# Optimization experiments

Measured on AMD Instinct MI355X. Metric: run time of the kernel, lower is better.

## Reference

```python
import jax, jax.numpy as jnp
import numpy as np

N, M, L, D = 8, 32, 256, 768
H = 4 * D  # mlp hidden
EPS = 1e-5


def setup_inputs() -> dict:
    key = jax.random.key(0)
    ks = jax.random.split(key, 8)
    s = 0.02
    return {
        "x": jax.random.normal(ks[0], (N, M, L, D), jnp.float32),
        "probe": jax.random.normal(ks[1], (1, 1, 1, D), jnp.float32) * s,
        "wq": jax.random.normal(ks[2], (D, D), jnp.float32) * s,
        "bq": jnp.zeros((D,), jnp.float32),
        "wk": jax.random.normal(ks[3], (D, D), jnp.float32) * s,
        "bk": jnp.zeros((D,), jnp.float32),
        "wv": jax.random.normal(ks[4], (D, D), jnp.float32) * s,
        "bv": jnp.zeros((D,), jnp.float32),
        "gamma": jnp.ones((D,), jnp.float32),
        "beta": jnp.zeros((D,), jnp.float32),
        "w1": jax.random.normal(ks[5], (H, D), jnp.float32) * s,
        "b1": jnp.zeros((H,), jnp.float32),
        "w2": jax.random.normal(ks[6], (D, H), jnp.float32) * s,
        "b2": jnp.zeros((D,), jnp.float32),
    }


def _layernorm(x, gamma, beta):
    mu = jnp.mean(x, axis=-1, keepdims=True)
    var = jnp.var(x, axis=-1, keepdims=True)
    return (x - mu) * jax.lax.rsqrt(var + EPS) * gamma + beta


def reference(x, probe, wq, bq, wk, bk, wv, bv, gamma, beta, w1, b1, w2, b2):
    n, m, l, d = x.shape
    # probe is tiled over (n, m); the query projection is identical per (n, m),
    # so compute it once: (1,1,q,d) -> (q,d)
    q = probe[0, 0] @ wq.T + bq                      # (q, d)
    k = x @ wk.T + bk                                # (n, m, l, d)
    v = x @ wv.T + bv                                # (n, m, l, d)
    att = jnp.einsum('qd,nmkd->nmqk', q, k)          # (n, m, q, l)
    att = jax.nn.softmax(att / jnp.sqrt(jnp.float32(d)), axis=-1)
    xo = jnp.einsum('nmqk,nmkd->nmqd', att, v)       # (n, m, q, d)
    y = _layernorm(xo, gamma, beta)
    h = jax.nn.gelu(y @ w1.T + b1, approximate=False)
    out = xo + (h @ w2.T + b2)
    return out[:, :, 0, :]                           # (n, m, d)
```

## Files before the change

### kernel.cpp

```cpp
#include <hip/hip_runtime.h>
#include <math.h>

#define D_ 768
#define H_ 3072
#define L_ 256
#define NM_ 256
#define EPS_ 1e-5f
#define SCALE_ 0.036084391824351615f

__device__ __forceinline__ float wave_sum(float v) {
#pragma unroll
  for (int o = 32; o; o >>= 1) v += __shfl_down(v, o);
  return v;
}

__global__ __launch_bounds__(256) void k_qproj(const float* __restrict__ probe,
                                               const float* __restrict__ wq,
                                               const float* __restrict__ bq,
                                               float* __restrict__ q_out) {
  __shared__ float pr[D_];
  int t = threadIdx.x;
  for (int i = t; i < D_; i += 256) pr[i] = probe[i];
  __syncthreads();
  int wave = t >> 6, lane = t & 63;
  int row0 = blockIdx.x * 64 + wave * 16;
  for (int rr = 0; rr < 16; ++rr) {
    int row = row0 + rr;
    const float4* wrow = (const float4*)(wq + (size_t)row * D_);
    const float4* prow = (const float4*)pr;
    float acc = 0.f;
#pragma unroll
    for (int it = 0; it < 3; ++it) {
      float4 w4 = wrow[it * 64 + lane];
      float4 p4 = prow[it * 64 + lane];
      acc += w4.x * p4.x + w4.y * p4.y + w4.z * p4.z + w4.w * p4.w;
    }
    acc = wave_sum(acc);
    if (lane == 0) q_out[row] = (acc + bq[row]) * SCALE_;
  }
}

__global__ __launch_bounds__(256) void k_kproj(const float* __restrict__ q,
                                               const float* __restrict__ wk,
                                               const float* __restrict__ bk,
                                               float* __restrict__ qkp,
                                               float* __restrict__ biasp) {
  __shared__ float qs[192];
  __shared__ float red[256];
  int t = threadIdx.x;
  int c = blockIdx.x, ks = blockIdx.y;
  int jbase = 192 * ks;
  if (t < 192) qs[t] = q[jbase + t];
  __syncthreads();
  int d = c * 256 + t;
  float acc = 0.f;
  for (int jj = 0; jj < 192; ++jj) acc += qs[jj] * wk[(size_t)(jbase + jj) * D_ + d];
  qkp[ks * D_ + d] = acc;
  if (c == 0) {
    float s = (t < 192) ? qs[t] * bk[jbase + t] : 0.f;
    red[t] = s;
    __syncthreads();
    for (int o = 128; o; o >>= 1) {
      if (t < o) red[t] += red[t + o];
      __syncthreads();
    }
    if (t == 0) biasp[ks] = red[0];
  }
}

#define CHUNK_ 16
__global__ __launch_bounds__(256) void k_attnpool(const float* __restrict__ x,
                                                  const float* __restrict__ qkp,
                                                  const float* __restrict__ biasp,
                                                  float* __restrict__ pooledP,
                                                  float2* __restrict__ mlP) {
  __shared__ float xs[CHUNK_][D_];
  __shared__ float qk_s[D_];
  __shared__ float sc_s[CHUNK_];
  __shared__ float red[4][D_];
  int t = threadIdx.x, wave = t >> 6, lane = t & 63;
  int nm = blockIdx.x, part = blockIdx.y;
  const float* xb = x + (size_t)nm * L_ * D_ + (size_t)part * (L_ / 2) * D_;
  for (int i = t; i < D_; i += 256)
    qk_s[i] = qkp[i] + qkp[D_ + i] + qkp[2 * D_ + i] + qkp[3 * D_ + i];
  float ab = biasp[0] + biasp[1] + biasp[2] + biasp[3];

  float m_run = -1e30f, l_run = 0.f;
  float acc[3][4];
#pragma unroll
  for (int it = 0; it < 3; ++it)
#pragma unroll
    for (int c = 0; c < 4; ++c) acc[it][c] = 0.f;

  const float4* qk4 = (const float4*)qk_s;

  for (int ch = 0; ch < (L_ / 2) / CHUNK_; ++ch) {
    __syncthreads();
    {
      const float4* src = (const float4*)(xb + (size_t)ch * CHUNK_ * D_);
      float4* dstv = (float4*)&xs[0][0];
      for (int i = t; i < CHUNK_ * (D_ / 4); i += 256) dstv[i] = src[i];
    }
    __syncthreads();
#pragma unroll
    for (int qq = 0; qq < 4; ++qq) {
      int rr = 4 * wave + qq;
      const float4* xr = (const float4*)&xs[rr][0];
      float a = 0.f;
#pragma unroll
      for (int it = 0; it < 3; ++it) {
        float4 xv = xr[it * 64 + lane];
        float4 qv = qk4[it * 64 + lane];
        a += xv.x * qv.x + xv.y * qv.y + xv.z * qv.z + xv.w * qv.w;
      }
      a = wave_sum(a);
      if (lane == 0) sc_s[rr] = a + ab;
    }
    __syncthreads();
    float mx = m_run;
#pragma unroll
    for (int i = 0; i < CHUNK_; ++i) mx = fmaxf(mx, sc_s[i]);
    float factor = expf(m_run - mx);
    float psum = 0.f;
#pragma unroll
    for (int i = 0; i < CHUNK_; ++i) psum += expf(sc_s[i] - mx);
    l_run = l_run * factor + psum;
    m_run = mx;
#pragma unroll
    for (int it = 0; it < 3; ++it)
#pragma unroll
      for (int c = 0; c < 4; ++c) acc[it][c] *= factor;
#pragma unroll
    for (int qq = 0; qq < 4; ++qq) {
      int rr = 4 * wave + qq;
      float pq = expf(sc_s[rr] - mx);
      const float4* xr = (const float4*)&xs[rr][0];
#pragma unroll
      for (int it = 0; it < 3; ++it) {
        float4 xv = xr[it * 64 + lane];
        acc[it][0] += pq * xv.x;
        acc[it][1] += pq * xv.y;
        acc[it][2] += pq * xv.z;
        acc[it][3] += pq * xv.w;
      }
    }
  }
#pragma unroll
  for (int it = 0; it < 3; ++it) {
    float4 v = make_float4(acc[it][0], acc[it][1], acc[it][2], acc[it][3]);
    *(float4*)&red[wave][it * 256 + 4 * lane] = v;
  }
  __syncthreads();
#pragma unroll
  for (int it = 0; it < 3; ++it) {
    int dd = t + it * 256;
    pooledP[((size_t)part * NM_ + nm) * D_ + dd] =
        red[0][dd] + red[1][dd] + red[2][dd] + red[3][dd];
  }
  if (t == 0) mlP[part * NM_ + nm] = make_float2(m_run, l_run);
}

__global__ __launch_bounds__(256) void k_merge(float* __restrict__ pooledP,
                                               const float2* __restrict__ mlP) {
  int t = threadIdx.x, nm = blockIdx.x;
  float2 a = mlP[nm], b = mlP[NM_ + nm];
  float M = fmaxf(a.x, b.x);
  float wa = expf(a.x - M), wb = expf(b.x - M);
  float inv = 1.f / (wa * a.y + wb * b.y);
#pragma unroll
  for (int it = 0; it < 3; ++it) {
    int d = t + it * 256;
    size_t ia = (size_t)nm * D_ + d;
    size_t ib = (size_t)(NM_ + nm) * D_ + d;
    pooledP[ia] = (wa * pooledP[ia] + wb * pooledP[ib]) * inv;
  }
}

__global__ __launch_bounds__(256) void k_gemm(const float* __restrict__ A, int K,
                                              const float* __restrict__ W,
                                              float* __restrict__ Cp, int N, int kchunk) {
  __shared__ float A_s[64][36];
  __shared__ float B_s[32][68];
  int t = threadIdx.x;
  int tx = t & 15, ty = t >> 4;
  int n0 = blockIdx.x * 64, m0 = blockIdx.y * 64;
  int k0 = blockIdx.z * kchunk;
  float4 acc[4];
#pragma unroll
  for (int u = 0; u < 4; ++u) acc[u] = make_float4(0.f, 0.f, 0.f, 0.f);

  for (int kc = 0; kc < kchunk; kc += 32) {
    __syncthreads();
#pragma unroll
    for (int it = 0; it < 2; ++it) {
      int idx = t + it * 256;
      int row = idx >> 3, c4 = idx & 7;
      float4 v = *(const float4*)&A[(size_t)(m0 + row) * K + k0 + kc + 4 * c4];
      *(float4*)&A_s[row][4 * c4] = v;
      float4 w = *(const float4*)&W[(size_t)(n0 + row) * K + k0 + kc + 4 * c4];
      B_s[4 * c4 + 0][row] = w.x;
      B_s[4 * c4 + 1][row] = w.y;
      B_s[4 * c4 + 2][row] = w.z;
      B_s[4 * c4 + 3][row] = w.w;
    }
    __syncthreads();
#pragma unroll
    for (int kk = 0; kk < 32; ++kk) {
      float4 b4 = *(const float4*)&B_s[kk][tx * 4];
      float a0 = A_s[ty * 4 + 0][kk];
      float a1 = A_s[ty * 4 + 1][kk];
      float a2 = A_s[ty * 4 + 2][kk];
      float a3 = A_s[ty * 4 + 3][kk];
      acc[0].x += a0 * b4.x; acc[0].y += a0 * b4.y; acc[0].z += a0 * b4.z; acc[0].w += a0 * b4.w;
      acc[1].x += a1 * b4.x; acc[1].y += a1 * b4.y; acc[1].z += a1 * b4.z; acc[1].w += a1 * b4.w;
      acc[2].x += a2 * b4.x; acc[2].y += a2 * b4.y; acc[2].z += a2 * b4.z; acc[2].w += a2 * b4.w;
      acc[3].x += a3 * b4.x; acc[3].y += a3 * b4.y; acc[3].z += a3 * b4.z; acc[3].w += a3 * b4.w;
    }
  }
  size_t base = (size_t)blockIdx.z * NM_ * N;
#pragma unroll
  for (int u = 0; u < 4; ++u)
    *(float4*)&Cp[base + (size_t)(m0 + ty * 4 + u) * N + n0 + tx * 4] = acc[u];
}

__global__ __launch_bounds__(256) void k_ep1(const float* __restrict__ xop,
                                             const float* __restrict__ bv,
                                             const float* __restrict__ gamma,
                                             const float* __restrict__ beta,
                                             float* __restrict__ xo,
                                             float* __restrict__ y) {
  __shared__ float tmpa[4], tmpb[4];
  int t = threadIdx.x, wave = t >> 6, lane = t & 63;
  int row = blockIdx.x;
  float v[3];
#pragma unroll
  for (int cc = 0; cc < 3; ++cc) {
    int j = t + 256 * cc;
    float s = bv[j];
#pragma unroll
    for (int p = 0; p < 6; ++p) s += xop[(size_t)p * NM_ * D_ + (size_t)row * D_ + j];
    v[cc] = s;
    xo[(size_t)row * D_ + j] = s;
  }
  float s = v[0] + v[1] + v[2];
  float ss = v[0] * v[0] + v[1] * v[1] + v[2] * v[2];
#pragma unroll
  for (int o = 32; o; o >>= 1) {
    s += __shfl_down(s, o);
    ss += __shfl_down(ss, o);
  }
  if (lane == 0) { tmpa[wave] = s; tmpb[wave] = ss; }
  __syncthreads();
  float mu = (tmpa[0] + tmpa[1] + tmpa[2] + tmpa[3]) * (1.f / D_);
  float var = (tmpb[0] + tmpb[1] + tmpb[2] + tmpb[3]) * (1.f / D_) - mu * mu;
  float rs = rsqrtf(var + EPS_);
#pragma unroll
  for (int cc = 0; cc < 3; ++cc) {
    int j = t + 256 * cc;
    y[(size_t)row * D_ + j] = (v[cc] - mu) * rs * gamma[j] + beta[j];
  }
}

__global__ __launch_bounds__(256) void k_ep2(const float* __restrict__ hp,
                                             const float* __restrict__ b1,
                                             float* __restrict__ h) {
  int idx4 = blockIdx.x * 256 + threadIdx.x;
  int f = idx4 * 4;
  int col = f % H_;
  float4 p0 = *(const float4*)&hp[f];
  float4 p1 = *(const float4*)&hp[(size_t)NM_ * H_ + f];
  float4 bb = *(const float4*)&b1[col];
  float4 r;
  float vx = p0.x + p1.x + bb.x;
  float vy = p0.y + p1.y + bb.y;
  float vz = p0.z + p1.z + bb.z;
  float vw = p0.w + p1.w + bb.w;
  r.x = 0.5f * vx * (1.f + erff(vx * 0.70710678118f));
  r.y = 0.5f * vy * (1.f + erff(vy * 0.70710678118f));
  r.z = 0.5f * vz * (1.f + erff(vz * 0.70710678118f));
  r.w = 0.5f * vw * (1.f + erff(vw * 0.70710678118f));
  *(float4*)&h[f] = r;
}

__global__ __launch_bounds__(256) void k_ep3(const float* __restrict__ op,
                                             const float* __restrict__ b2,
                                             const float* __restrict__ xo,
                                             float* __restrict__ out) {
  int idx4 = blockIdx.x * 256 + threadIdx.x;
  int f = idx4 * 4;
  int col = f % D_;
  float4 bb = *(const float4*)&b2[col];
  float4 xv = *(const float4*)&xo[f];
  float sx = bb.x + xv.x, sy = bb.y + xv.y, sz = bb.z + xv.z, sw = bb.w + xv.w;
#pragma unroll
  for (int p = 0; p < 8; ++p) {
    float4 pv = *(const float4*)&op[(size_t)p * NM_ * D_ + f];
    sx += pv.x; sy += pv.y; sz += pv.z; sw += pv.w;
  }
  *(float4*)&out[f] = make_float4(sx, sy, sz, sw);
}

extern "C" void kernel_launch(void* const* d_in, const int* in_sizes, int n_in,
                              void* d_out, int out_size, void* d_ws, size_t ws_size,
                              hipStream_t stream) {
  const float* x = (const float*)d_in[0];
  const float* probe = (const float*)d_in[1];
  const float* wq = (const float*)d_in[2];
  const float* bq = (const float*)d_in[3];
  const float* wk = (const float*)d_in[4];
  const float* bk = (const float*)d_in[5];
  const float* wv = (const float*)d_in[6];
  const float* bv = (const float*)d_in[7];
  const float* gamma = (const float*)d_in[8];
  const float* beta = (const float*)d_in[9];
  const float* w1 = (const float*)d_in[10];
  const float* b1 = (const float*)d_in[11];
  const float* w2 = (const float*)d_in[12];
  const float* b2 = (const float*)d_in[13];
  float* out = (float*)d_out;

  float* ws = (float*)d_ws;
  float* qkp = ws;
  float* biasp = ws + 3072;
  float* q = ws + 3104;
  float* pooledP = ws + 4096;
  float2* mlP = (float2*)(ws + 397312);
  float* xop = ws + 398336;
  float* xo = ws + 1577984;
  float* y = ws + 1774592;
  float* hp = ws + 1971200;
  float* h = ws + 3544064;
  float* op = ws + 4330496;

  hipLaunchKernelGGL(k_qproj, dim3(12), dim3(256), 0, stream, probe, wq, bq, q);
  hipLaunchKernelGGL(k_kproj, dim3(3, 4), dim3(256), 0, stream, q, wk, bk, qkp, biasp);
  hipLaunchKernelGGL(k_attnpool, dim3(NM_, 2), dim3(256), 0, stream, x, qkp, biasp, pooledP, mlP);
  hipLaunchKernelGGL(k_merge, dim3(NM_), dim3(256), 0, stream, pooledP, mlP);
  hipLaunchKernelGGL(k_gemm, dim3(12, 4, 6), dim3(256), 0, stream, pooledP, D_, wv, xop, D_, 128);
  hipLaunchKernelGGL(k_ep1, dim3(NM_), dim3(256), 0, stream, xop, bv, gamma, beta, xo, y);
  hipLaunchKernelGGL(k_gemm, dim3(48, 4, 2), dim3(256), 0, stream, y, D_, w1, hp, H_, 384);
  hipLaunchKernelGGL(k_ep2, dim3(768), dim3(256), 0, stream, hp, b1, h);
  hipLaunchKernelGGL(k_gemm, dim3(12, 4, 8), dim3(256), 0, stream, h, H_, w2, op, D_, 384);
  hipLaunchKernelGGL(k_ep3, dim3(192), dim3(256), 0, stream, op, b2, xo, out);
}
```

Before: 441.7 us.

## Switch MLP GEMMs to bf16 MFMA, fuse epilogues, prefetch x in attention pooling

Replaces the fp32 SIMT GEMMs with bf16 MFMA 16x16x32 GEMMs. The weights are cast to bf16 on every call and the activations are stored as bf16. The bias and GELU epilogues are fused into the GEMMs, which removes most split-K partial buffers. The q and k projections are merged into one kernel, and the constant bk bias term is dropped because softmax ignores it. The attention-pool loop now register-prefetches the next x chunk. The costs are reduced precision and a weight-cast kernel on every call.

```diff
diff --git a/kernel.cpp b/kernel.cpp
--- a/kernel.cpp
+++ b/kernel.cpp
@@ -8,82 +8,89 @@
 #define EPS_ 1e-5f
 #define SCALE_ 0.036084391824351615f
 
+typedef __attribute__((ext_vector_type(8))) short short8v;
+typedef __attribute__((ext_vector_type(4))) float f4v;
+
 __device__ __forceinline__ float wave_sum(float v) {
 #pragma unroll
   for (int o = 32; o; o >>= 1) v += __shfl_down(v, o);
   return v;
 }
 
-__global__ __launch_bounds__(256) void k_qproj(const float* __restrict__ probe,
-                                               const float* __restrict__ wq,
-                                               const float* __restrict__ bq,
-                                               float* __restrict__ q_out) {
+__device__ __forceinline__ unsigned short f2bf(float f) {
+  unsigned int u = __float_as_uint(f);
+  return (unsigned short)((u + 0x7FFFu + ((u >> 16) & 1u)) >> 16);
+}
+
+__global__ __launch_bounds__(256) void k_cast(const float* __restrict__ s0,
+                                              const float* __restrict__ s1,
+                                              const float* __restrict__ s2,
+                                              short* __restrict__ d0,
+                                              short* __restrict__ d1,
+                                              short* __restrict__ d2) {
+  const float* s;
+  short* d;
+  int sz;
+  if (blockIdx.y == 0) { s = s0; d = d0; sz = D_ * D_; }
+  else if (blockIdx.y == 1) { s = s1; d = d1; sz = H_ * D_; }
+  else { s = s2; d = d2; sz = D_ * H_; }
+  int base = blockIdx.x * 1024 + threadIdx.x * 4;
+  if (base >= sz) return;
+  float4 v = *(const float4*)&s[base];
+  short4 r;
+  r.x = (short)f2bf(v.x); r.y = (short)f2bf(v.y);
+  r.z = (short)f2bf(v.z); r.w = (short)f2bf(v.w);
+  *(short4*)&d[base] = r;
+}
+
+__global__ __launch_bounds__(256) void k_qk(const float* __restrict__ probe,
+                                            const float* __restrict__ wq,
+                                            const float* __restrict__ bq,
+                                            const float* __restrict__ wk,
+                                            float* __restrict__ qk) {
   __shared__ float pr[D_];
+  __shared__ float qs[D_];
+  __shared__ float part[4][64];
   int t = threadIdx.x;
   for (int i = t; i < D_; i += 256) pr[i] = probe[i];
   __syncthreads();
-  int wave = t >> 6, lane = t & 63;
-  int row0 = blockIdx.x * 64 + wave * 16;
-  for (int rr = 0; rr < 16; ++rr) {
-    int row = row0 + rr;
-    const float4* wrow = (const float4*)(wq + (size_t)row * D_);
-    const float4* prow = (const float4*)pr;
+#pragma unroll
+  for (int rr = 0; rr < 3; ++rr) {
+    int r = t + rr * 256;
+    const float4* w4 = (const float4*)(wq + (size_t)r * D_);
+    const float4* p4 = (const float4*)pr;
     float acc = 0.f;
-#pragma unroll
-    for (int it = 0; it < 3; ++it) {
-      float4 w4 = wrow[it * 64 + lane];
-      float4 p4 = prow[it * 64 + lane];
-      acc += w4.x * p4.x + w4.y * p4.y + w4.z * p4.z + w4.w * p4.w;
-    }
-    acc = wave_sum(acc);
-    if (lane == 0) q_out[row] = (acc + bq[row]) * SCALE_;
-  }
-}
-
-__global__ __launch_bounds__(256) void k_kproj(const float* __restrict__ q,
-                                               const float* __restrict__ wk,
-                                               const float* __restrict__ bk,
-                                               float* __restrict__ qkp,
-                                               float* __restrict__ biasp) {
-  __shared__ float qs[192];
-  __shared__ float red[256];
-  int t = threadIdx.x;
-  int c = blockIdx.x, ks = blockIdx.y;
-  int jbase = 192 * ks;
-  if (t < 192) qs[t] = q[jbase + t];
-  __syncthreads();
-  int d = c * 256 + t;
+    for (int i = 0; i < 192; ++i) {
+      float4 a = w4[i], b = p4[i];
+      acc += a.x * b.x + a.y * b.y + a.z * b.z + a.w * b.w;
+    }
+    qs[r] = (acc + bq[r]) * SCALE_;
+  }
+  __syncthreads();
+  int col = blockIdx.x * 64 + (t & 63);
+  int wv_ = t >> 6;
   float acc = 0.f;
-  for (int jj = 0; jj < 192; ++jj) acc += qs[jj] * wk[(size_t)(jbase + jj) * D_ + d];
-  qkp[ks * D_ + d] = acc;
-  if (c == 0) {
-    float s = (t < 192) ? qs[t] * bk[jbase + t] : 0.f;
-    red[t] = s;
-    __syncthreads();
-    for (int o = 128; o; o >>= 1) {
-      if (t < o) red[t] += red[t + o];
-      __syncthreads();
-    }
-    if (t == 0) biasp[ks] = red[0];
-  }
+  for (int j = wv_ * 192; j < wv_ * 192 + 192; ++j) acc += qs[j] * wk[(size_t)j * D_ + col];
+  part[wv_][t & 63] = acc;
+  __syncthreads();
+  if (t < 64) qk[blockIdx.x * 64 + t] = part[0][t] + part[1][t] + part[2][t] + part[3][t];
 }
 
 #define CHUNK_ 16
+#define NCH_ 8
 __global__ __launch_bounds__(256) void k_attnpool(const float* __restrict__ x,
-                                                  const float* __restrict__ qkp,
-                                                  const float* __restrict__ biasp,
+                                                  const float* __restrict__ qk,
                                                   float* __restrict__ pooledP,
                                                   float2* __restrict__ mlP) {
   __shared__ float xs[CHUNK_][D_];
-  __shared__ float qk_s[D_];
   __shared__ float sc_s[CHUNK_];
   __shared__ float red[4][D_];
   int t = threadIdx.x, wave = t >> 6, lane = t & 63;
   int nm = blockIdx.x, part = blockIdx.y;
   const float* xb = x + (size_t)nm * L_ * D_ + (size_t)part * (L_ / 2) * D_;
-  for (int i = t; i < D_; i += 256)
-    qk_s[i] = qkp[i] + qkp[D_ + i] + qkp[2 * D_ + i] + qkp[3 * D_ + i];
-  float ab = biasp[0] + biasp[1] + biasp[2] + biasp[3];
+  float4 qr[3];
+#pragma unroll
+  for (int it = 0; it < 3; ++it) qr[it] = *(const float4*)&qk[(it * 64 + lane) * 4];
 
   float m_run = -1e30f, l_run = 0.f;
   float acc[3][4];
@@ -92,16 +99,26 @@
 #pragma unroll
     for (int c = 0; c < 4; ++c) acc[it][c] = 0.f;
 
-  const float4* qk4 = (const float4*)qk_s;
-
-  for (int ch = 0; ch < (L_ / 2) / CHUNK_; ++ch) {
+  float4 pf[12];
+  {
+    const float4* src = (const float4*)xb;
+#pragma unroll
+    for (int i = 0; i < 12; ++i) pf[i] = src[t + i * 256];
+  }
+
+  for (int ch = 0; ch < NCH_; ++ch) {
     __syncthreads();
     {
-      const float4* src = (const float4*)(xb + (size_t)ch * CHUNK_ * D_);
       float4* dstv = (float4*)&xs[0][0];
-      for (int i = t; i < CHUNK_ * (D_ / 4); i += 256) dstv[i] = src[i];
+#pragma unroll
+      for (int i = 0; i < 12; ++i) dstv[t + i * 256] = pf[i];
     }
     __syncthreads();
+    if (ch + 1 < NCH_) {
+      const float4* nsrc = (const float4*)(xb + (size_t)(ch + 1) * CHUNK_ * D_);
+#pragma unroll
+      for (int i = 0; i < 12; ++i) pf[i] = nsrc[t + i * 256];
+    }
 #pragma unroll
     for (int qq = 0; qq < 4; ++qq) {
       int rr = 4 * wave + qq;
@@ -110,11 +127,10 @@
 #pragma unroll
       for (int it = 0; it < 3; ++it) {
         float4 xv = xr[it * 64 + lane];
-        float4 qv = qk4[it * 64 + lane];
-        a += xv.x * qv.x + xv.y * qv.y + xv.z * qv.z + xv.w * qv.w;
+        a += xv.x * qr[it].x + xv.y * qr[it].y + xv.z * qr[it].z + xv.w * qr[it].w;
       }
       a = wave_sum(a);
-      if (lane == 0) sc_s[rr] = a + ab;
+      if (lane == 0) sc_s[rr] = a;
     }
     __syncthreads();
     float mx = m_run;
@@ -146,10 +162,9 @@
     }
   }
 #pragma unroll
-  for (int it = 0; it < 3; ++it) {
-    float4 v = make_float4(acc[it][0], acc[it][1], acc[it][2], acc[it][3]);
-    *(float4*)&red[wave][it * 256 + 4 * lane] = v;
-  }
+  for (int it = 0; it < 3; ++it)
+    *(float4*)&red[wave][it * 256 + 4 * lane] =
+        make_float4(acc[it][0], acc[it][1], acc[it][2], acc[it][3]);
   __syncthreads();
 #pragma unroll
   for (int it = 0; it < 3; ++it) {
@@ -160,8 +175,9 @@
   if (t == 0) mlP[part * NM_ + nm] = make_float2(m_run, l_run);
 }
 
-__global__ __launch_bounds__(256) void k_merge(float* __restrict__ pooledP,
-                                               const float2* __restrict__ mlP) {
+__global__ __launch_bounds__(256) void k_merge(const float* __restrict__ pooledP,
+                                               const float2* __restrict__ mlP,
+                                               short* __restrict__ pooled_bf) {
   int t = threadIdx.x, nm = blockIdx.x;
   float2 a = mlP[nm], b = mlP[NM_ + nm];
   float M = fmaxf(a.x, b.x);
@@ -170,78 +186,108 @@
 #pragma unroll
   for (int it = 0; it < 3; ++it) {
     int d = t + it * 256;
-    size_t ia = (size_t)nm * D_ + d;
-    size_t ib = (size_t)(NM_ + nm) * D_ + d;
-    pooledP[ia] = (wa * pooledP[ia] + wb * pooledP[ib]) * inv;
-  }
-}
-
-__global__ __launch_bounds__(256) void k_gemm(const float* __restrict__ A, int K,
-                                              const float* __restrict__ W,
-                                              float* __restrict__ Cp, int N, int kchunk) {
-  __shared__ float A_s[64][36];
-  __shared__ float B_s[32][68];
-  int t = threadIdx.x;
-  int tx = t & 15, ty = t >> 4;
-  int n0 = blockIdx.x * 64, m0 = blockIdx.y * 64;
-  int k0 = blockIdx.z * kchunk;
-  float4 acc[4];
-#pragma unroll
-  for (int u = 0; u < 4; ++u) acc[u] = make_float4(0.f, 0.f, 0.f, 0.f);
-
-  for (int kc = 0; kc < kchunk; kc += 32) {
-    __syncthreads();
-#pragma unroll
-    for (int it = 0; it < 2; ++it) {
-      int idx = t + it * 256;
-      int row = idx >> 3, c4 = idx & 7;
-      float4 v = *(const float4*)&A[(size_t)(m0 + row) * K + k0 + kc + 4 * c4];
-      *(float4*)&A_s[row][4 * c4] = v;
-      float4 w = *(const float4*)&W[(size_t)(n0 + row) * K + k0 + kc + 4 * c4];
-      B_s[4 * c4 + 0][row] = w.x;
-      B_s[4 * c4 + 1][row] = w.y;
-      B_s[4 * c4 + 2][row] = w.z;
-      B_s[4 * c4 + 3][row] = w.w;
-    }
-    __syncthreads();
-#pragma unroll
-    for (int kk = 0; kk < 32; ++kk) {
-      float4 b4 = *(const float4*)&B_s[kk][tx * 4];
-      float a0 = A_s[ty * 4 + 0][kk];
-      float a1 = A_s[ty * 4 + 1][kk];
-      float a2 = A_s[ty * 4 + 2][kk];
-      float a3 = A_s[ty * 4 + 3][kk];
-      acc[0].x += a0 * b4.x; acc[0].y += a0 * b4.y; acc[0].z += a0 * b4.z; acc[0].w += a0 * b4.w;
-      acc[1].x += a1 * b4.x; acc[1].y += a1 * b4.y; acc[1].z += a1 * b4.z; acc[1].w += a1 * b4.w;
-      acc[2].x += a2 * b4.x; acc[2].y += a2 * b4.y; acc[2].z += a2 * b4.z; acc[2].w += a2 * b4.w;
-      acc[3].x += a3 * b4.x; acc[3].y += a3 * b4.y; acc[3].z += a3 * b4.z; acc[3].w += a3 * b4.w;
-    }
-  }
-  size_t base = (size_t)blockIdx.z * NM_ * N;
-#pragma unroll
-  for (int u = 0; u < 4; ++u)
-    *(float4*)&Cp[base + (size_t)(m0 + ty * 4 + u) * N + n0 + tx * 4] = acc[u];
-}
-
-__global__ __launch_bounds__(256) void k_ep1(const float* __restrict__ xop,
-                                             const float* __restrict__ bv,
+    float v = (wa * pooledP[(size_t)nm * D_ + d] + wb * pooledP[(size_t)(NM_ + nm) * D_ + d]) * inv;
+    pooled_bf[(size_t)nm * D_ + d] = (short)f2bf(v);
+  }
+}
+
+#define GEMM_PROLOG(Kval)                                                            \
+  __shared__ short A_s[64 * 40];                                                     \
+  __shared__ short W_s[64 * 40];                                                     \
+  int t = threadIdx.x, wave = t >> 6, lane = t & 63;                                 \
+  int wr = wave >> 1, wc = wave & 1;                                                 \
+  int fr = lane & 15, fh = lane >> 4;                                                \
+  int n0 = blockIdx.x * 64, m0 = blockIdx.y * 64;                                    \
+  int srow = t >> 2, sseg = t & 3;                                                   \
+  f4v accv[2][2];                                                                    \
+  accv[0][0] = (f4v){0.f, 0.f, 0.f, 0.f}; accv[0][1] = (f4v){0.f, 0.f, 0.f, 0.f};   \
+  accv[1][0] = (f4v){0.f, 0.f, 0.f, 0.f}; accv[1][1] = (f4v){0.f, 0.f, 0.f, 0.f};
+
+#define GEMM_KLOOP(Abf, Wbf, Kval, k0val, NSTEP)                                     \
+  for (int ks = 0; ks < (NSTEP); ++ks) {                                             \
+    __syncthreads();                                                                 \
+    *(float4*)&A_s[srow * 40 + sseg * 8] =                                           \
+        *(const float4*)&(Abf)[(size_t)(m0 + srow) * (Kval) + (k0val) + ks * 32 + sseg * 8]; \
+    *(float4*)&W_s[srow * 40 + sseg * 8] =                                           \
+        *(const float4*)&(Wbf)[(size_t)(n0 + srow) * (Kval) + (k0val) + ks * 32 + sseg * 8]; \
+    __syncthreads();                                                                 \
+    short8v a0 = *(short8v*)&A_s[(wr * 32 + fr) * 40 + fh * 8];                      \
+    short8v a1 = *(short8v*)&A_s[(wr * 32 + 16 + fr) * 40 + fh * 8];                 \
+    short8v b0 = *(short8v*)&W_s[(wc * 32 + fr) * 40 + fh * 8];                      \
+    short8v b1 = *(short8v*)&W_s[(wc * 32 + 16 + fr) * 40 + fh * 8];                 \
+    accv[0][0] = __builtin_amdgcn_mfma_f32_16x16x32_bf16(a0, b0, accv[0][0], 0, 0, 0); \
+    accv[0][1] = __builtin_amdgcn_mfma_f32_16x16x32_bf16(a0, b1, accv[0][1], 0, 0, 0); \
+    accv[1][0] = __builtin_amdgcn_mfma_f32_16x16x32_bf16(a1, b0, accv[1][0], 0, 0, 0); \
+    accv[1][1] = __builtin_amdgcn_mfma_f32_16x16x32_bf16(a1, b1, accv[1][1], 0, 0, 0); \
+  }
+
+__global__ __launch_bounds__(256) void k_gemm_xo(const short* __restrict__ Abf,
+                                                 const short* __restrict__ Wbf,
+                                                 const float* __restrict__ bv,
+                                                 float* __restrict__ xo) {
+  GEMM_PROLOG(D_)
+  GEMM_KLOOP(Abf, Wbf, D_, 0, 24)
+#pragma unroll
+  for (int mi = 0; mi < 2; ++mi)
+#pragma unroll
+    for (int ni = 0; ni < 2; ++ni)
+#pragma unroll
+      for (int r = 0; r < 4; ++r) {
+        int row = m0 + wr * 32 + mi * 16 + fh * 4 + r;
+        int col = n0 + wc * 32 + ni * 16 + fr;
+        xo[(size_t)row * D_ + col] = accv[mi][ni][r] + bv[col];
+      }
+}
+
+__global__ __launch_bounds__(256) void k_gemm_gelu(const short* __restrict__ Abf,
+                                                   const short* __restrict__ Wbf,
+                                                   const float* __restrict__ b1,
+                                                   short* __restrict__ h_bf) {
+  GEMM_PROLOG(D_)
+  GEMM_KLOOP(Abf, Wbf, D_, 0, 24)
+#pragma unroll
+  for (int mi = 0; mi < 2; ++mi)
+#pragma unroll
+    for (int ni = 0; ni < 2; ++ni)
+#pragma unroll
+      for (int r = 0; r < 4; ++r) {
+        int row = m0 + wr * 32 + mi * 16 + fh * 4 + r;
+        int col = n0 + wc * 32 + ni * 16 + fr;
+        float v = accv[mi][ni][r] + b1[col];
+        float g = 0.5f * v * (1.f + erff(v * 0.70710678118f));
+        h_bf[(size_t)row * H_ + col] = (short)f2bf(g);
+      }
+}
+
+__global__ __launch_bounds__(256) void k_gemm_o(const short* __restrict__ Abf,
+                                                const short* __restrict__ Wbf,
+                                                float* __restrict__ op) {
+  GEMM_PROLOG(H_)
+  int k0 = blockIdx.z * 768;
+  GEMM_KLOOP(Abf, Wbf, H_, k0, 24)
+  float* dst = op + (size_t)blockIdx.z * NM_ * D_;
+#pragma unroll
+  for (int mi = 0; mi < 2; ++mi)
+#pragma unroll
+    for (int ni = 0; ni < 2; ++ni)
+#pragma unroll
+      for (int r = 0; r < 4; ++r) {
+        int row = m0 + wr * 32 + mi * 16 + fh * 4 + r;
+        int col = n0 + wc * 32 + ni * 16 + fr;
+        dst[(size_t)row * D_ + col] = accv[mi][ni][r];
+      }
+}
+
+__global__ __launch_bounds__(256) void k_ep1(const float* __restrict__ xo,
                                              const float* __restrict__ gamma,
                                              const float* __restrict__ beta,
-                                             float* __restrict__ xo,
-                                             float* __restrict__ y) {
+                                             short* __restrict__ y_bf) {
   __shared__ float tmpa[4], tmpb[4];
   int t = threadIdx.x, wave = t >> 6, lane = t & 63;
   int row = blockIdx.x;
   float v[3];
 #pragma unroll
-  for (int cc = 0; cc < 3; ++cc) {
-    int j = t + 256 * cc;
-    float s = bv[j];
-#pragma unroll
-    for (int p = 0; p < 6; ++p) s += xop[(size_t)p * NM_ * D_ + (size_t)row * D_ + j];
-    v[cc] = s;
-    xo[(size_t)row * D_ + j] = s;
-  }
+  for (int cc = 0; cc < 3; ++cc) v[cc] = xo[(size_t)row * D_ + t + 256 * cc];
   float s = v[0] + v[1] + v[2];
   float ss = v[0] * v[0] + v[1] * v[1] + v[2] * v[2];
 #pragma unroll
@@ -257,43 +303,21 @@
 #pragma unroll
   for (int cc = 0; cc < 3; ++cc) {
     int j = t + 256 * cc;
-    y[(size_t)row * D_ + j] = (v[cc] - mu) * rs * gamma[j] + beta[j];
-  }
-}
-
-__global__ __launch_bounds__(256) void k_ep2(const float* __restrict__ hp,
-                                             const float* __restrict__ b1,
-                                             float* __restrict__ h) {
-  int idx4 = blockIdx.x * 256 + threadIdx.x;
-  int f = idx4 * 4;
-  int col = f % H_;
-  float4 p0 = *(const float4*)&hp[f];
-  float4 p1 = *(const float4*)&hp[(size_t)NM_ * H_ + f];
-  float4 bb = *(const float4*)&b1[col];
-  float4 r;
-  float vx = p0.x + p1.x + bb.x;
-  float vy = p0.y + p1.y + bb.y;
-  float vz = p0.z + p1.z + bb.z;
-  float vw = p0.w + p1.w + bb.w;
-  r.x = 0.5f * vx * (1.f + erff(vx * 0.70710678118f));
-  r.y = 0.5f * vy * (1.f + erff(vy * 0.70710678118f));
-  r.z = 0.5f * vz * (1.f + erff(vz * 0.70710678118f));
-  r.w = 0.5f * vw * (1.f + erff(vw * 0.70710678118f));
-  *(float4*)&h[f] = r;
+    y_bf[(size_t)row * D_ + j] = (short)f2bf((v[cc] - mu) * rs * gamma[j] + beta[j]);
+  }
 }
 
 __global__ __launch_bounds__(256) void k_ep3(const float* __restrict__ op,
                                              const float* __restrict__ b2,
                                              const float* __restrict__ xo,
                                              float* __restrict__ out) {
-  int idx4 = blockIdx.x * 256 + threadIdx.x;
-  int f = idx4 * 4;
+  int f = (blockIdx.x * 256 + threadIdx.x) * 4;
   int col = f % D_;
   float4 bb = *(const float4*)&b2[col];
   float4 xv = *(const float4*)&xo[f];
   float sx = bb.x + xv.x, sy = bb.y + xv.y, sz = bb.z + xv.z, sw = bb.w + xv.w;
 #pragma unroll
-  for (int p = 0; p < 8; ++p) {
+  for (int p = 0; p < 4; ++p) {
     float4 pv = *(const float4*)&op[(size_t)p * NM_ * D_ + f];
     sx += pv.x; sy += pv.y; sz += pv.z; sw += pv.w;
   }
@@ -308,7 +332,6 @@
   const float* wq = (const float*)d_in[2];
   const float* bq = (const float*)d_in[3];
   const float* wk = (const float*)d_in[4];
-  const float* bk = (const float*)d_in[5];
   const float* wv = (const float*)d_in[6];
   const float* bv = (const float*)d_in[7];
   const float* gamma = (const float*)d_in[8];
@@ -320,26 +343,25 @@
   float* out = (float*)d_out;
 
   float* ws = (float*)d_ws;
-  float* qkp = ws;
-  float* biasp = ws + 3072;
-  float* q = ws + 3104;
-  float* pooledP = ws + 4096;
-  float2* mlP = (float2*)(ws + 397312);
-  float* xop = ws + 398336;
-  float* xo = ws + 1577984;
-  float* y = ws + 1774592;
-  float* hp = ws + 1971200;
-  float* h = ws + 3544064;
-  float* op = ws + 4330496;
-
-  hipLaunchKernelGGL(k_qproj, dim3(12), dim3(256), 0, stream, probe, wq, bq, q);
-  hipLaunchKernelGGL(k_kproj, dim3(3, 4), dim3(256), 0, stream, q, wk, bk, qkp, biasp);
-  hipLaunchKernelGGL(k_attnpool, dim3(NM_, 2), dim3(256), 0, stream, x, qkp, biasp, pooledP, mlP);
-  hipLaunchKernelGGL(k_merge, dim3(NM_), dim3(256), 0, stream, pooledP, mlP);
-  hipLaunchKernelGGL(k_gemm, dim3(12, 4, 6), dim3(256), 0, stream, pooledP, D_, wv, xop, D_, 128);
-  hipLaunchKernelGGL(k_ep1, dim3(NM_), dim3(256), 0, stream, xop, bv, gamma, beta, xo, y);
-  hipLaunchKernelGGL(k_gemm, dim3(48, 4, 2), dim3(256), 0, stream, y, D_, w1, hp, H_, 384);
-  hipLaunchKernelGGL(k_ep2, dim3(768), dim3(256), 0, stream, hp, b1, h);
-  hipLaunchKernelGGL(k_gemm, dim3(12, 4, 8), dim3(256), 0, stream, h, H_, w2, op, D_, 384);
+  float* qk = ws;
+  float2* mlP = (float2*)(ws + 768);
+  float* pooledP = ws + 2048;
+  float* xo = ws + 395264;
+  float* op = ws + 591872;
+  short* pooled_bf = (short*)(ws + 1378304);
+  short* y_bf = (short*)(ws + 1476608);
+  short* h_bf = (short*)(ws + 1574912);
+  short* wv_bf = (short*)(ws + 1968128);
+  short* w1_bf = (short*)(ws + 2263040);
+  short* w2_bf = (short*)(ws + 3442688);
+
+  hipLaunchKernelGGL(k_cast, dim3(2304, 3), dim3(256), 0, stream, wv, w1, w2, wv_bf, w1_bf, w2_bf);
+  hipLaunchKernelGGL(k_qk, dim3(12), dim3(256), 0, stream, probe, wq, bq, wk, qk);
+  hipLaunchKernelGGL(k_attnpool, dim3(NM_, 2), dim3(256), 0, stream, x, qk, pooledP, mlP);
+  hipLaunchKernelGGL(k_merge, dim3(NM_), dim3(256), 0, stream, pooledP, mlP, pooled_bf);
+  hipLaunchKernelGGL(k_gemm_xo, dim3(12, 4), dim3(256), 0, stream, pooled_bf, wv_bf, bv, xo);
+  hipLaunchKernelGGL(k_ep1, dim3(NM_), dim3(256), 0, stream, xo, gamma, beta, y_bf);
+  hipLaunchKernelGGL(k_gemm_gelu, dim3(48, 4), dim3(256), 0, stream, y_bf, w1_bf, b1, h_bf);
+  hipLaunchKernelGGL(k_gemm_o, dim3(12, 4, 4), dim3(256), 0, stream, h_bf, w2_bf, op);
   hipLaunchKernelGGL(k_ep3, dim3(192), dim3(256), 0, stream, op, b2, xo, out);
 }
```

After: 488.0 us. 1.1x slower.
